# Kernel tuning notes

Hardware: AMD Instinct MI355X
Metric: run time of the kernel (lower is better)

Reference implementation:

```python
import jax, jax.numpy as jnp
import numpy as np


def ternary_quantize(t, threshold, scale):
    # values in {-scale, 0, +scale}
    return jnp.where(t > threshold, scale, jnp.where(t < -threshold, -scale, 0.0)).astype(t.dtype)


def setup_inputs() -> dict:
    key = jax.random.key(0)
    k1, k2, k3 = jax.random.split(key, 3)
    B, S, D = 4, 4096, 2048  # batch, seq, d_model (in=out=D)
    x = jax.random.normal(k1, (B, S, D), dtype=jnp.float32)
    weight = jax.random.normal(k2, (D, D), dtype=jnp.float32) * 0.02
    # layer_name == 'query' -> gaussian RRAM variation (std chosen as 0.05, mean 0)
    rram_variation = jax.random.normal(k3, (D, D), dtype=jnp.float32) * 0.05
    return {"x": x, "weight": weight, "rram_variation": rram_variation}


def reference(x, weight, rram_variation):
    TH_X, SC_X = 0.33, 0.5      # activation ternary threshold/scale
    TH_W, SC_W = 0.2, 0.6       # weight ternary threshold (th_value) / scale (clamp_value)
    x_q = ternary_quantize(x, TH_X, SC_X)                 # [B,S,D]
    w_q = ternary_quantize(weight, TH_W, SC_W)            # [O,D]
    w_rram = w_q + rram_variation                         # [O,D]
    # F.linear: x_q @ w_rram.T, no bias
    return jnp.einsum('bsd,od->bso', x_q, w_rram)
```

## Files before the change

### kernel.cpp

```cpp
#include <hip/hip_runtime.h>
#include <hip/hip_bf16.h>
#include <cmath>
#include <cstdint>


#define AS1 __attribute__((address_space(1)))
#define AS3 __attribute__((address_space(3)))

typedef unsigned short u16;
typedef __bf16 bf16x8 __attribute__((ext_vector_type(8)));
typedef float f32x4 __attribute__((ext_vector_type(4)));
typedef unsigned short u16x4 __attribute__((ext_vector_type(4)));

#define BM 256
#define BN 256
#define BK 32
#define NBUF 4

__device__ __forceinline__ u16 f2bf_rne(float f) {
  uint32_t u = __float_as_uint(f);
  u += 0x7FFFu + ((u >> 16) & 1u);
  return (u16)(u >> 16);
}

__device__ __forceinline__ u16 ter_x(float v) {
  double d = (double)v;
  return d > 0.33 ? (u16)0x3F00u : (d < -0.33 ? (u16)0xBF00u : (u16)0u);
}

__device__ __forceinline__ float ter_w(float v) {
  double d = (double)v;
  return d > 0.2 ? 0.6f : (d < -0.2 ? -0.6f : 0.0f);
}

__global__ void quant_x_kernel(const float* __restrict__ x, u16* __restrict__ xq,
                               long n4) {
  long i = (long)blockIdx.x * blockDim.x + threadIdx.x;
  if (i >= n4) return;
  float4 v = ((const float4*)x)[i];
  u16x4 q;
  q.x = ter_x(v.x); q.y = ter_x(v.y); q.z = ter_x(v.z); q.w = ter_x(v.w);
  ((u16x4*)xq)[i] = q;
}

__global__ void quant_w_kernel(const float* __restrict__ w,
                               const float* __restrict__ rr,
                               u16* __restrict__ wq, long n4) {
  long i = (long)blockIdx.x * blockDim.x + threadIdx.x;
  if (i >= n4) return;
  float4 a = ((const float4*)w)[i];
  float4 b = ((const float4*)rr)[i];
  u16x4 q;
  q.x = f2bf_rne(ter_w(a.x) + b.x);
  q.y = f2bf_rne(ter_w(a.y) + b.y);
  q.z = f2bf_rne(ter_w(a.z) + b.z);
  q.w = f2bf_rne(ter_w(a.w) + b.w);
  ((u16x4*)wq)[i] = q;
}

__device__ __forceinline__ void gld_lds16(const void* g, void* l) {
  __builtin_amdgcn_global_load_lds((AS1 void*)g, (AS3 void*)l, 16, 0, 0);
}

__global__ __launch_bounds__(512, 2) void gemm256_kernel(
    const u16* __restrict__ Aq, const u16* __restrict__ Bq,
    float* __restrict__ C, int M, int N, int K) {
  __shared__ u16 lds[NBUF * 16384];

  const int tid  = threadIdx.x;
  const int wid  = tid >> 6;
  const int lane = tid & 63;
  const int wm = wid >> 2;
  const int wn = wid & 3;

  const int m0 = blockIdx.y * BM;
  const int n0 = blockIdx.x * BN;

  const int srow = wid * 16 + (lane >> 2);
  const int scol = ((lane & 3) * 8) ^ ((lane & 32) ? 16 : 0);
  const u16* pa = Aq + (size_t)(m0 + srow) * K + scol;
  const u16* pb = Bq + (size_t)(n0 + srow) * K + scol;
  const size_t slot1 = (size_t)128 * K;
  const int sd = wid * 512;

  const int fr  = lane & 15;
  const int fk  = (lane >> 4) * 8;
  const int col = fk ^ ((fr & 8) ? 16 : 0);
  const int aoff = (wm * 128 + fr) * 32 + col;
  const int boff = 8192 + (wn * 64 + fr) * 32 + col;

  f32x4 acc[8][4] = {};
  const int nt = K / BK;

#pragma unroll
  for (int T = 0; T < 3; ++T) {
    const int bb = T * 16384;
    const u16* at = pa + (size_t)T * BK;
    const u16* bt = pb + (size_t)T * BK;
    gld_lds16(at,         &lds[bb + sd]);
    gld_lds16(at + slot1, &lds[bb + sd + 4096]);
    gld_lds16(bt,         &lds[bb + 8192 + sd]);
    gld_lds16(bt + slot1, &lds[bb + 8192 + sd + 4096]);
  }

  for (int t = 0; t < nt; ++t) {
    if (t < nt - 2)       asm volatile("s_waitcnt vmcnt(8)" ::: "memory");
    else if (t == nt - 2) asm volatile("s_waitcnt vmcnt(4)" ::: "memory");
    else                  asm volatile("s_waitcnt vmcnt(0)" ::: "memory");
    __builtin_amdgcn_sched_barrier(0);
    __builtin_amdgcn_s_barrier();
    __builtin_amdgcn_sched_barrier(0);

    const int rb = (t & 3) * 16384;
    const int Tn = t + 3;
    const int bb = (Tn & 3) * 16384;
    const u16* at = pa + (size_t)Tn * BK;
    const u16* bt = pb + (size_t)Tn * BK;

    bf16x8 a[8], b[4];

#pragma unroll
    for (int i = 0; i < 4; ++i) a[i] = *(const bf16x8*)&lds[rb + aoff + i * 512];
#pragma unroll
    for (int j = 0; j < 4; ++j) b[j] = *(const bf16x8*)&lds[rb + boff + j * 512];
    if (Tn < nt) {
      gld_lds16(at,         &lds[bb + sd]);
      gld_lds16(at + slot1, &lds[bb + sd + 4096]);
    }
    asm volatile("s_waitcnt lgkmcnt(0)" ::: "memory");
    __builtin_amdgcn_sched_barrier(0);
    __builtin_amdgcn_s_setprio(1);
#pragma unroll
    for (int i = 0; i < 4; ++i)
#pragma unroll
      for (int j = 0; j < 4; ++j)
        acc[i][j] =
            __builtin_amdgcn_mfma_f32_16x16x32_bf16(a[i], b[j], acc[i][j], 0, 0, 0);
    __builtin_amdgcn_s_setprio(0);
    __builtin_amdgcn_sched_barrier(0);
    __builtin_amdgcn_s_barrier();
    __builtin_amdgcn_sched_barrier(0);

#pragma unroll
    for (int i = 4; i < 8; ++i) a[i] = *(const bf16x8*)&lds[rb + aoff + i * 512];
    if (Tn < nt) {
      gld_lds16(bt,         &lds[bb + 8192 + sd]);
      gld_lds16(bt + slot1, &lds[bb + 8192 + sd + 4096]);
    }
    asm volatile("s_waitcnt lgkmcnt(0)" ::: "memory");
    __builtin_amdgcn_sched_barrier(0);
    __builtin_amdgcn_s_setprio(1);
#pragma unroll
    for (int i = 4; i < 8; ++i)
#pragma unroll
      for (int j = 0; j < 4; ++j)
        acc[i][j] =
            __builtin_amdgcn_mfma_f32_16x16x32_bf16(a[i], b[j], acc[i][j], 0, 0, 0);
    __builtin_amdgcn_s_setprio(0);
    __builtin_amdgcn_sched_barrier(0);
  }

  const int om = m0 + wm * 128 + (lane >> 4) * 4;
  const int on = n0 + wn * 64 + (lane & 15);
#pragma unroll
  for (int i = 0; i < 8; ++i)
#pragma unroll
    for (int j = 0; j < 4; ++j)
#pragma unroll
      for (int r = 0; r < 4; ++r)
        C[(size_t)(om + i * 16 + r) * N + (on + j * 16)] = acc[i][j][r];
}

__global__ __launch_bounds__(256) void gemm_fused128_kernel(
    const float* __restrict__ Xf, const u16* __restrict__ Bq,
    float* __restrict__ C, int M, int N, int K) {
  __shared__ u16 As[128 * 64];
  __shared__ u16 Bs[128 * 64];

  const int tid  = threadIdx.x;
  const int wid  = tid >> 6;
  const int lane = tid & 63;
  const int m0 = blockIdx.y * 128;
  const int n0 = blockIdx.x * 128;
  const int r8 = lane >> 3;
  const int c8 = (lane & 7) * 8;
  const int mw = (wid >> 1) * 64;
  const int nw = (wid & 1) * 64;
  const int fr = lane & 15;
  const int fk = (lane >> 4) * 8;

  f32x4 acc[4][4] = {};

  for (int k0 = 0; k0 < K; k0 += 64) {
#pragma unroll
    for (int t = 0; t < 4; ++t) {
      const int rbase = wid * 32 + t * 8;
      gld_lds16(Bq + (size_t)(n0 + rbase + r8) * K + k0 + c8, &Bs[rbase * 64]);
    }
#pragma unroll
    for (int it = 0; it < 8; ++it) {
      const int idx = it * 256 + tid;
      const int row = idx >> 4;
      const int c4  = (idx & 15) * 4;
      const float4 v = *(const float4*)&Xf[(size_t)(m0 + row) * K + k0 + c4];
      u16x4 q;
      q.x = ter_x(v.x); q.y = ter_x(v.y); q.z = ter_x(v.z); q.w = ter_x(v.w);
      *(u16x4*)&As[row * 64 + c4] = q;
    }
    __syncthreads();

#pragma unroll
    for (int kk = 0; kk < 64; kk += 32) {
      bf16x8 a[4], b[4];
#pragma unroll
      for (int i = 0; i < 4; ++i)
        a[i] = *(const bf16x8*)&As[(mw + i * 16 + fr) * 64 + kk + fk];
#pragma unroll
      for (int j = 0; j < 4; ++j)
        b[j] = *(const bf16x8*)&Bs[(nw + j * 16 + fr) * 64 + kk + fk];
#pragma unroll
      for (int i = 0; i < 4; ++i)
#pragma unroll
        for (int j = 0; j < 4; ++j)
          acc[i][j] =
              __builtin_amdgcn_mfma_f32_16x16x32_bf16(a[i], b[j], acc[i][j], 0, 0, 0);
    }
    __syncthreads();
  }

  const int om = m0 + mw + (lane >> 4) * 4;
  const int on = n0 + nw + (lane & 15);
#pragma unroll
  for (int i = 0; i < 4; ++i)
#pragma unroll
    for (int j = 0; j < 4; ++j)
#pragma unroll
      for (int r = 0; r < 4; ++r)
        C[(size_t)(om + i * 16 + r) * N + (on + j * 16)] = acc[i][j][r];
}

extern "C" void kernel_launch(void* const* d_in, const int* in_sizes, int n_in,
                              void* d_out, int out_size, void* d_ws, size_t ws_size,
                              hipStream_t stream) {
  const float* x  = (const float*)d_in[0];
  const float* w  = (const float*)d_in[1];
  const float* rr = (const float*)d_in[2];
  float* out = (float*)d_out;

  const long xn = (long)in_sizes[0];
  const long wn = (long)in_sizes[1];
  const int K = (int)llround(std::sqrt((double)wn));
  const int N = K;
  const int M = (int)(xn / K);

  u16* wq = (u16*)d_ws;
  u16* xq = (u16*)d_ws + (size_t)N * K;
  const size_t need = ((size_t)M * K + (size_t)N * K) * sizeof(u16);

  {
    long n4 = wn / 4;
    quant_w_kernel<<<(int)((n4 + 255) / 256), 256, 0, stream>>>(w, rr, wq, n4);
  }

  const bool ok256 = (M % BM == 0) && (N % BN == 0) && (K % BK == 0) &&
                     (K / BK >= 4) && (ws_size >= need);
  if (ok256) {
    long n4 = xn / 4;
    quant_x_kernel<<<(int)((n4 + 255) / 256), 256, 0, stream>>>(x, xq, n4);
    dim3 grid(N / BN, M / BM);
    gemm256_kernel<<<grid, 512, 0, stream>>>(xq, wq, out, M, N, K);
  } else {
    dim3 grid(N / 128, M / 128);
    gemm_fused128_kernel<<<grid, 256, 0, stream>>>(x, wq, out, M, N, K);
  }
}
```

Baseline: 363.3 us.

## Software-pipeline LDS fragment loads with MFMA and use single barrier per K-step

Restructures the 256x256 GEMM main loop so that LDS fragment reads for A are interleaved in pairs with MFMA groups, and the B fragments plus first A fragments of the next tile are prefetched after the barrier. It reduces prefetch depth from three tiles to two and drops the mid-iteration barrier, leaving one barrier per K-step. The aim is to hide LDS latency behind matrix ops and cut synchronization overhead. In exchange, the shallower global prefetch may expose more memory latency, and relying on compiler waitcnt insertion for the interleaved LDS reads is fragile.

```diff
diff --git a/kernel.cpp b/kernel.cpp
--- a/kernel.cpp
+++ b/kernel.cpp
@@ -93,7 +93,7 @@
   const int nt = K / BK;
 
 #pragma unroll
-  for (int T = 0; T < 3; ++T) {
+  for (int T = 0; T < 2; ++T) {
     const int bb = T * 16384;
     const u16* at = pa + (size_t)T * BK;
     const u16* bt = pb + (size_t)T * BK;
@@ -102,61 +102,91 @@
     gld_lds16(bt,         &lds[bb + 8192 + sd]);
     gld_lds16(bt + slot1, &lds[bb + 8192 + sd + 4096]);
   }
+  asm volatile("s_waitcnt vmcnt(4)" ::: "memory");
+  __builtin_amdgcn_sched_barrier(0);
+  __builtin_amdgcn_s_barrier();
+  __builtin_amdgcn_sched_barrier(0);
+
+  bf16x8 ag[8], bg[4];
+#pragma unroll
+  for (int j = 0; j < 4; ++j) bg[j] = *(const bf16x8*)&lds[boff + j * 512];
+  ag[0] = *(const bf16x8*)&lds[aoff];
+  ag[1] = *(const bf16x8*)&lds[aoff + 512];
 
   for (int t = 0; t < nt; ++t) {
-    if (t < nt - 2)       asm volatile("s_waitcnt vmcnt(8)" ::: "memory");
-    else if (t == nt - 2) asm volatile("s_waitcnt vmcnt(4)" ::: "memory");
-    else                  asm volatile("s_waitcnt vmcnt(0)" ::: "memory");
-    __builtin_amdgcn_sched_barrier(0);
-    __builtin_amdgcn_s_barrier();
-    __builtin_amdgcn_sched_barrier(0);
-
     const int rb = (t & 3) * 16384;
-    const int Tn = t + 3;
-    const int bb = (Tn & 3) * 16384;
-    const u16* at = pa + (size_t)Tn * BK;
-    const u16* bt = pb + (size_t)Tn * BK;
-
-    bf16x8 a[8], b[4];
-
-#pragma unroll
-    for (int i = 0; i < 4; ++i) a[i] = *(const bf16x8*)&lds[rb + aoff + i * 512];
-#pragma unroll
-    for (int j = 0; j < 4; ++j) b[j] = *(const bf16x8*)&lds[rb + boff + j * 512];
-    if (Tn < nt) {
+
+    if (t + 2 < nt) {
+      const int bb = ((t + 2) & 3) * 16384;
+      const u16* at = pa + (size_t)(t + 2) * BK;
+      const u16* bt = pb + (size_t)(t + 2) * BK;
       gld_lds16(at,         &lds[bb + sd]);
       gld_lds16(at + slot1, &lds[bb + sd + 4096]);
-    }
-    asm volatile("s_waitcnt lgkmcnt(0)" ::: "memory");
-    __builtin_amdgcn_sched_barrier(0);
-    __builtin_amdgcn_s_setprio(1);
-#pragma unroll
-    for (int i = 0; i < 4; ++i)
-#pragma unroll
-      for (int j = 0; j < 4; ++j)
-        acc[i][j] =
-            __builtin_amdgcn_mfma_f32_16x16x32_bf16(a[i], b[j], acc[i][j], 0, 0, 0);
-    __builtin_amdgcn_s_setprio(0);
-    __builtin_amdgcn_sched_barrier(0);
-    __builtin_amdgcn_s_barrier();
-    __builtin_amdgcn_sched_barrier(0);
-
-#pragma unroll
-    for (int i = 4; i < 8; ++i) a[i] = *(const bf16x8*)&lds[rb + aoff + i * 512];
-    if (Tn < nt) {
       gld_lds16(bt,         &lds[bb + 8192 + sd]);
       gld_lds16(bt + slot1, &lds[bb + 8192 + sd + 4096]);
     }
-    asm volatile("s_waitcnt lgkmcnt(0)" ::: "memory");
+    __builtin_amdgcn_sched_barrier(0);
+
+    ag[2] = *(const bf16x8*)&lds[rb + aoff + 2 * 512];
+    ag[3] = *(const bf16x8*)&lds[rb + aoff + 3 * 512];
     __builtin_amdgcn_sched_barrier(0);
     __builtin_amdgcn_s_setprio(1);
 #pragma unroll
-    for (int i = 4; i < 8; ++i)
-#pragma unroll
-      for (int j = 0; j < 4; ++j)
-        acc[i][j] =
-            __builtin_amdgcn_mfma_f32_16x16x32_bf16(a[i], b[j], acc[i][j], 0, 0, 0);
+    for (int j = 0; j < 4; ++j)
+      acc[0][j] = __builtin_amdgcn_mfma_f32_16x16x32_bf16(ag[0], bg[j], acc[0][j], 0, 0, 0);
+#pragma unroll
+    for (int j = 0; j < 4; ++j)
+      acc[1][j] = __builtin_amdgcn_mfma_f32_16x16x32_bf16(ag[1], bg[j], acc[1][j], 0, 0, 0);
     __builtin_amdgcn_s_setprio(0);
+    __builtin_amdgcn_sched_barrier(0);
+
+    ag[4] = *(const bf16x8*)&lds[rb + aoff + 4 * 512];
+    ag[5] = *(const bf16x8*)&lds[rb + aoff + 5 * 512];
+    __builtin_amdgcn_sched_barrier(0);
+    __builtin_amdgcn_s_setprio(1);
+#pragma unroll
+    for (int j = 0; j < 4; ++j)
+      acc[2][j] = __builtin_amdgcn_mfma_f32_16x16x32_bf16(ag[2], bg[j], acc[2][j], 0, 0, 0);
+#pragma unroll
+    for (int j = 0; j < 4; ++j)
+      acc[3][j] = __builtin_amdgcn_mfma_f32_16x16x32_bf16(ag[3], bg[j], acc[3][j], 0, 0, 0);
+    __builtin_amdgcn_s_setprio(0);
+    __builtin_amdgcn_sched_barrier(0);
+
+    ag[6] = *(const bf16x8*)&lds[rb + aoff + 6 * 512];
+    ag[7] = *(const bf16x8*)&lds[rb + aoff + 7 * 512];
+    __builtin_amdgcn_sched_barrier(0);
+    __builtin_amdgcn_s_setprio(1);
+#pragma unroll
+    for (int j = 0; j < 4; ++j)
+      acc[4][j] = __builtin_amdgcn_mfma_f32_16x16x32_bf16(ag[4], bg[j], acc[4][j], 0, 0, 0);
+#pragma unroll
+    for (int j = 0; j < 4; ++j)
+      acc[5][j] = __builtin_amdgcn_mfma_f32_16x16x32_bf16(ag[5], bg[j], acc[5][j], 0, 0, 0);
+    __builtin_amdgcn_s_setprio(0);
+    __builtin_amdgcn_sched_barrier(0);
+    __builtin_amdgcn_s_setprio(1);
+#pragma unroll
+    for (int j = 0; j < 4; ++j)
+      acc[6][j] = __builtin_amdgcn_mfma_f32_16x16x32_bf16(ag[6], bg[j], acc[6][j], 0, 0, 0);
+#pragma unroll
+    for (int j = 0; j < 4; ++j)
+      acc[7][j] = __builtin_amdgcn_mfma_f32_16x16x32_bf16(ag[7], bg[j], acc[7][j], 0, 0, 0);
+    __builtin_amdgcn_s_setprio(0);
+    __builtin_amdgcn_sched_barrier(0);
+
+    if (t < nt - 2) asm volatile("s_waitcnt vmcnt(4)" ::: "memory");
+    else            asm volatile("s_waitcnt vmcnt(0)" ::: "memory");
+    __builtin_amdgcn_sched_barrier(0);
+    __builtin_amdgcn_s_barrier();
+    __builtin_amdgcn_sched_barrier(0);
+    if (t + 1 < nt) {
+      const int rb2 = ((t + 1) & 3) * 16384;
+#pragma unroll
+      for (int j = 0; j < 4; ++j) bg[j] = *(const bf16x8*)&lds[rb2 + boff + j * 512];
+      ag[0] = *(const bf16x8*)&lds[rb2 + aoff];
+      ag[1] = *(const bf16x8*)&lds[rb2 + aoff + 512];
+    }
     __builtin_amdgcn_sched_barrier(0);
   }
 
```

After: 358.2 us. No clear change (-1.4%).
